# Kernel tuning notes

Hardware: AMD Instinct MI355X
Metric: run time of the kernel (lower is better)

## Reference

```python
import jax, jax.numpy as jnp
import numpy as np

LEBESGUE_P = 3          # lebesgue_p from __init__
WEIGHT_RANGE = 0.1      # weight init scale
B, C_IN, H, W = 32, 96, 56, 56
C_OUT, K = 384, 3
STRIDE = (1, 1)
PADDING = ((1, 1), (1, 1))


def setup_inputs() -> dict:
    key = jax.random.key(0)
    kx, kw = jax.random.split(key)
    x = jax.random.normal(kx, (B, C_IN, H, W), dtype=jnp.float32)
    # learned buffer 'weight': [out_channels, in_channels, kH, kW]
    weight = jax.random.normal(kw, (C_OUT, C_IN, K, K), dtype=jnp.float32) * WEIGHT_RANGE
    return {"x": x, "weight": weight}


def reference(x, weight):
    # get_pre_activations: conv with power-transformed weight sign(w)*|w|^(p-1)
    w_eff = jnp.sign(weight) * jnp.abs(weight) ** (LEBESGUE_P - 1)
    pre_x = jax.lax.conv_general_dilated(
        x, w_eff,
        window_strides=STRIDE,
        padding=PADDING,
        dimension_numbers=("NCHW", "OIHW", "NCHW"),
    )  # [B, C_OUT, H, W]

    # get_wta (groups=1): hard winner-take-all over channel dim per (b, h, w).
    # Original transposes/reshapes to [C_OUT, B*H*W], argmax over dim 0, one_hot,
    # then reshapes back; mathematically identical to a channel-axis argmax+one_hot.
    winners = jnp.argmax(pre_x, axis=1)                                   # [B, H, W]
    wta = jax.nn.one_hot(winners, pre_x.shape[1], axis=1, dtype=pre_x.dtype)  # [B, C_OUT, H, W]

    # forward(x, return_x_wta=True) returns (pre_x, wta); stack so output is one array
    return jnp.stack([pre_x, wta], axis=0)  # [2, B, C_OUT, H, W]
```

## Files before the change

### kernel.cpp

```cpp
#include <hip/hip_runtime.h>
#include <math.h>
#include <stdint.h>

#define CIN  96
#define COUT 384
#define HH   56
#define WW   56
#define BB   32

#define MARGIN   1e-3f
#define CAP      32000u
#define WT32_OFF (256 * 1024)
#define WT64_OFF (2 * 1024 * 1024)
#define WT16_OFF (5 * 1024 * 1024)
#define POSB     4

#define HL2      331776
#define XSB      6336

typedef _Float16 half8 __attribute__((ext_vector_type(8)));
typedef float    f32x4 __attribute__((ext_vector_type(4)));

template <bool WITH16>
__global__ void prep_weights(const float* __restrict__ w, float* __restrict__ wt32,
                             double* __restrict__ wt64, _Float16* __restrict__ wt16,
                             uint32_t* __restrict__ cnt) {
    int idx = blockIdx.x * blockDim.x + threadIdx.x;
    if (idx == 0) *cnt = 0u;
    if (idx >= COUT * CIN * 9) return;
    int co = idx / (CIN * 9);
    int r  = idx - co * (CIN * 9);
    double d = (double)w[idx];
    double e = d * fabs(d);
    wt64[(size_t)r * COUT + co] = e;
    float ef = (float)e;
    wt32[(size_t)r * COUT + co] = ef;
    if (WITH16) {
        _Float16 hi = (_Float16)ef;
        _Float16 lo = (_Float16)(ef - (float)hi);
        int ci  = r / 9;
        int khw = r - ci * 9;
        int off = (((co >> 4) * 12 + (ci >> 3)) * 9 + khw) * 128 + (co & 15) * 8 + (ci & 7);
        wt16[off] = hi;
        wt16[off + HL2] = lo;
    }
}

__global__ __launch_bounds__(512, 4)
void conv_mfma(const float* __restrict__ x, const _Float16* __restrict__ wt16,
               float* __restrict__ out, uint32_t* __restrict__ cnt,
               uint32_t* __restrict__ flags) {
    const int h   = blockIdx.x;
    const int b   = blockIdx.y;
    const int tid = threadIdx.x;
    const int l   = tid & 63;
    const int wg  = tid >> 6;
    const int g   = l >> 4;
    const int c   = l & 15;

    __shared__ char lds[33792];
    _Float16* xs  = (_Float16*)lds;
    float*    T   = (float*)lds;
    float4*   red = (float4*)(lds + 25344);
    int*      win = (int*)(lds + 25344 + 8192);

    f32x4 acc[4][3];
    #pragma unroll
    for (int mf = 0; mf < 4; ++mf)
        #pragma unroll
        for (int nf = 0; nf < 3; ++nf)
            #pragma unroll
            for (int q = 0; q < 4; ++q) acc[mf][nf][q] = 0.0f;

    const _Float16* pa0 = xs + (g * 198 + c) * 8;

    auto stage = [&](int chunk) {
        _Float16* xsb = xs + (chunk & 1) * XSB;
        const int ci0 = chunk * 32;
        for (int idx = tid; idx < 4 * 198; idx += 512) {
            int cq  = idx / 198;
            int rem = idx - cq * 198;
            int r   = rem / 66;
            int col = rem - r * 66;
            int gh  = h + r - 1;
            int gw  = col - 1;
            half8 hv = {};
            if ((unsigned)gh < 56u && (unsigned)gw < 56u) {
                const float* px = x + (((size_t)b * CIN + (ci0 + cq * 8)) * HH + gh) * WW + gw;
                #pragma unroll
                for (int i = 0; i < 8; ++i) hv[i] = (_Float16)px[i * 3136];
            }
            *(half8*)(xsb + (size_t)(cq * 198 + rem) * 8) = hv;
        }
    };

    stage(0);
    __syncthreads();

    for (int chunk = 0; chunk < 3; ++chunk) {
        if (chunk < 2) stage(chunk + 1);

        const _Float16* pax = pa0 + (chunk & 1) * XSB;
        const _Float16* pb0h = wt16 + (size_t)(((wg * 3 + 0) * 12 + chunk * 4 + g) * 9) * 128 + c * 8;
        const _Float16* pb1h = wt16 + (size_t)(((wg * 3 + 1) * 12 + chunk * 4 + g) * 9) * 128 + c * 8;
        const _Float16* pb2h = wt16 + (size_t)(((wg * 3 + 2) * 12 + chunk * 4 + g) * 9) * 128 + c * 8;
        const _Float16* pb0l = pb0h + HL2;
        const _Float16* pb1l = pb1h + HL2;
        const _Float16* pb2l = pb2h + HL2;

        #pragma unroll
        for (int khw = 0; khw < 9; ++khw) {
            const int kh = khw / 3;
            const int kw = khw - kh * 3;
            half8 Bh0 = *(const half8*)(pb0h + khw * 128);
            half8 Bl0 = *(const half8*)(pb0l + khw * 128);
            half8 Bh1 = *(const half8*)(pb1h + khw * 128);
            half8 Bl1 = *(const half8*)(pb1l + khw * 128);
            half8 Bh2 = *(const half8*)(pb2h + khw * 128);
            half8 Bl2 = *(const half8*)(pb2l + khw * 128);
            #pragma unroll
            for (int mf = 0; mf < 4; ++mf) {
                half8 Ah = *(const half8*)(pax + (kh * 66 + mf * 16 + kw) * 8);
                acc[mf][0] = __builtin_amdgcn_mfma_f32_16x16x32_f16(Ah, Bh0, acc[mf][0], 0, 0, 0);
                acc[mf][1] = __builtin_amdgcn_mfma_f32_16x16x32_f16(Ah, Bh1, acc[mf][1], 0, 0, 0);
                acc[mf][2] = __builtin_amdgcn_mfma_f32_16x16x32_f16(Ah, Bh2, acc[mf][2], 0, 0, 0);
                acc[mf][0] = __builtin_amdgcn_mfma_f32_16x16x32_f16(Ah, Bl0, acc[mf][0], 0, 0, 0);
                acc[mf][1] = __builtin_amdgcn_mfma_f32_16x16x32_f16(Ah, Bl1, acc[mf][1], 0, 0, 0);
                acc[mf][2] = __builtin_amdgcn_mfma_f32_16x16x32_f16(Ah, Bl2, acc[mf][2], 0, 0, 0);
            }
        }
        __syncthreads();
    }

    #pragma unroll
    for (int mf = 0; mf < 4; ++mf) {
        #pragma unroll
        for (int q = 0; q < 4; ++q) {
            float best = acc[mf][0][q];
            int   bco  = wg * 48 + c;
            float sec  = -1e30f;
            #pragma unroll
            for (int nf = 1; nf < 3; ++nf) {
                float v = acc[mf][nf][q];
                if (v > best) { sec = best; best = v; bco = wg * 48 + nf * 16 + c; }
                else if (v > sec) sec = v;
            }
            #pragma unroll
            for (int off = 1; off <= 8; off <<= 1) {
                float ov = __shfl_xor(best, off, 64);
                int   oc = __shfl_xor(bco,  off, 64);
                float os = __shfl_xor(sec,  off, 64);
                if (ov > best || (ov == best && oc < bco)) {
                    sec = fmaxf(best, os);
                    best = ov; bco = oc;
                } else {
                    sec = fmaxf(sec, ov);
                }
            }
            if (c == 0) {
                int m = mf * 16 + g * 4 + q;
                red[wg * 64 + m] = make_float4(best, sec, __int_as_float(bco), 0.0f);
            }
        }
    }
    __syncthreads();
    {
        const int m = tid >> 3;
        const int j = tid & 7;
        float4 v = red[j * 64 + m];
        float best = v.x, sec = v.y;
        int   bco  = __float_as_int(v.z);
        #pragma unroll
        for (int off = 1; off <= 4; off <<= 1) {
            float ov = __shfl_xor(best, off, 64);
            int   oc = __shfl_xor(bco,  off, 64);
            float os = __shfl_xor(sec,  off, 64);
            if (ov > best || (ov == best && oc < bco)) {
                sec = fmaxf(best, os);
                best = ov; bco = oc;
            } else {
                sec = fmaxf(sec, ov);
            }
        }
        if (j == 0 && m < 56) {
            win[m] = bco;
            if ((best - sec) < MARGIN) {
                uint32_t k = atomicAdd(cnt, 1u);
                if (k < CAP) flags[k] = (uint32_t)((b * 56 + h) * 56 + m);
            }
        }
    }
    __syncthreads();

    const size_t wta_off = (size_t)BB * COUT * HH * WW;
    for (int rnd = 0; rnd < 4; ++rnd) {
        if ((wg >> 1) == rnd) {
            const int wq = wg & 1;
            #pragma unroll
            for (int mf = 0; mf < 4; ++mf)
                #pragma unroll
                for (int nf = 0; nf < 3; ++nf)
                    #pragma unroll
                    for (int q = 0; q < 4; ++q)
                        T[(wq * 48 + nf * 16 + c) * 65 + mf * 16 + g * 4 + q] = acc[mf][nf][q];
        }
        __syncthreads();
        for (int t = tid; t < 96 * 64; t += 512) {
            int co_l = t >> 6;
            int m    = t & 63;
            if (m < 56) {
                int co  = rnd * 96 + co_l;
                float v = T[co_l * 65 + m];
                size_t o = ((size_t)(b * COUT + co)) * 3136 + (size_t)h * 56 + m;
                out[o] = v;
                out[wta_off + o] = (co == win[m]) ? 1.0f : 0.0f;
            }
        }
        __syncthreads();
    }
}

__global__ __launch_bounds__(512, 2)
void conv_wta_f32(const float* __restrict__ x, const float* __restrict__ wt,
                  float* __restrict__ out, uint32_t* __restrict__ cnt,
                  uint32_t* __restrict__ flags) {
    const int h0  = blockIdx.x * 2;
    const int b   = blockIdx.y;
    const int tid = threadIdx.x;
    const int cg  = tid & 63;
    const int wg  = tid >> 6;
    const int co0 = cg * 6;
    const int ws0 = wg * 7;

    __shared__ float xs[32 * 4 * 58];
    __shared__ int   win[2][56];

    float acc[2][6][7];
    #pragma unroll
    for (int r = 0; r < 2; ++r)
        #pragma unroll
        for (int c = 0; c < 6; ++c)
            #pragma unroll
            for (int i = 0; i < 7; ++i) acc[r][c][i] = 0.0f;

    for (int chunk = 0; chunk < 3; ++chunk) {
        const int ci0 = chunk * 32;
        __syncthreads();
        for (int idx = tid; idx < 32 * 4 * 58; idx += 512) {
            int ci  = idx / 232;
            int rem = idx - ci * 232;
            int r   = rem / 58;
            int c   = rem - r * 58;
            int gh  = h0 + r - 1;
            int gw  = c - 1;
            float v = 0.0f;
            if ((unsigned)gh < 56u && (unsigned)gw < 56u)
                v = x[(((size_t)b * CIN + (ci0 + ci)) * HH + gh) * WW + gw];
            xs[idx] = v;
        }
        __syncthreads();
        for (int ci = 0; ci < 32; ++ci) {
            const int gci = ci0 + ci;
            #pragma unroll
            for (int kh = 0; kh < 3; ++kh) {
                float xa[9], xb[9];
                const float* xr0 = &xs[(ci * 4 + kh) * 58 + ws0];
                const float* xr1 = &xs[(ci * 4 + kh + 1) * 58 + ws0];
                #pragma unroll
                for (int j = 0; j < 9; ++j) { xa[j] = xr0[j]; xb[j] = xr1[j]; }
                #pragma unroll
                for (int kw = 0; kw < 3; ++kw) {
                    const float* p = wt + (size_t)((gci * 3 + kh) * 3 + kw) * COUT + co0;
                    float2 w01 = *(const float2*)(p);
                    float2 w23 = *(const float2*)(p + 2);
                    float2 w45 = *(const float2*)(p + 4);
                    float wd[6] = {w01.x, w01.y, w23.x, w23.y, w45.x, w45.y};
                    #pragma unroll
                    for (int c = 0; c < 6; ++c)
                        #pragma unroll
                        for (int i = 0; i < 7; ++i) {
                            acc[0][c][i] = fmaf(wd[c], xa[i + kw], acc[0][c][i]);
                            acc[1][c][i] = fmaf(wd[c], xb[i + kw], acc[1][c][i]);
                        }
                }
            }
        }
    }

    #pragma unroll
    for (int rr = 0; rr < 2; ++rr) {
        #pragma unroll
        for (int i = 0; i < 7; ++i) {
            float best = acc[rr][0][i];
            int   bco  = co0;
            float sec  = -1e30f;
            #pragma unroll
            for (int c = 1; c < 6; ++c) {
                float v = acc[rr][c][i];
                if (v > best) { sec = best; best = v; bco = co0 + c; }
                else if (v > sec) sec = v;
            }
            #pragma unroll
            for (int off = 32; off > 0; off >>= 1) {
                float ov = __shfl_xor(best, off, 64);
                int   oc = __shfl_xor(bco,  off, 64);
                float os = __shfl_xor(sec,  off, 64);
                if (ov > best || (ov == best && oc < bco)) {
                    sec = fmaxf(best, os);
                    best = ov; bco = oc;
                } else {
                    sec = fmaxf(sec, ov);
                }
            }
            if (cg == 0) {
                win[rr][ws0 + i] = bco;
                if ((best - sec) < MARGIN) {
                    uint32_t k = atomicAdd(cnt, 1u);
                    if (k < CAP) flags[k] = (uint32_t)((b * 56 + (h0 + rr)) * 56 + (ws0 + i));
                }
            }
        }
    }

    const size_t wta_off = (size_t)BB * COUT * HH * WW;
    float* ldsT = xs;
    __syncthreads();
    for (int k = 0; k < 8; ++k) {
        if ((cg >> 3) == k) {
            const int cr = (cg & 7) * 6;
            #pragma unroll
            for (int c = 0; c < 6; ++c)
                #pragma unroll
                for (int rr = 0; rr < 2; ++rr)
                    #pragma unroll
                    for (int i = 0; i < 7; ++i)
                        ldsT[(cr + c) * 113 + rr * 56 + ws0 + i] = acc[rr][c][i];
        }
        __syncthreads();
        for (int l = tid; l < 48 * 112; l += 512) {
            int co_r = l / 112;
            int rem  = l - co_r * 112;
            int rr   = rem / 56;
            int w    = rem - rr * 56;
            int co   = k * 48 + co_r;
            float v  = ldsT[co_r * 113 + rem];
            size_t o = ((size_t)(b * COUT + co)) * 3136 + (size_t)(h0 + rr) * 56 + w;
            out[o] = v;
            out[wta_off + o] = (co == win[rr][w]) ? 1.0f : 0.0f;
        }
        __syncthreads();
    }
}

__global__ __launch_bounds__(384)
void fixup_f64(const float* __restrict__ x, const double* __restrict__ wt64,
               float* __restrict__ out, const uint32_t* __restrict__ cnt,
               const uint32_t* __restrict__ flags) {
    __shared__ double xp[POSB][CIN * 9];
    __shared__ double sv[POSB][COUT];
    __shared__ int winners[POSB];

    uint32_t n = *cnt;
    if (n > CAP) n = CAP;
    const int tid = threadIdx.x;
    const int wg  = tid >> 6;
    const int lane = tid & 63;
    const size_t wta_off = (size_t)BB * COUT * HH * WW;

    for (uint32_t base = blockIdx.x * POSB; base < n; base += gridDim.x * POSB) {
        int np = (int)(n - base) < POSB ? (int)(n - base) : POSB;
        __syncthreads();
        for (int idx = tid; idx < np * CIN * 9; idx += 384) {
            int p  = idx / (CIN * 9);
            int r  = idx - p * (CIN * 9);
            int ci = r / 9;
            int k  = r - ci * 9;
            int kh = k / 3, kw = k - kh * 3;
            uint32_t pos = flags[base + p];
            int w_ = pos % 56;
            int h_ = (pos / 56) % 56;
            int b_ = pos / 3136;
            int gh = h_ + kh - 1, gw = w_ + kw - 1;
            double v = 0.0;
            if ((unsigned)gh < 56u && (unsigned)gw < 56u)
                v = (double)x[(((size_t)b_ * CIN + ci) * HH + gh) * WW + gw];
            xp[p][r] = v;
        }
        __syncthreads();
        {
            const int co = tid;
            double a[POSB];
            #pragma unroll
            for (int p = 0; p < POSB; ++p) a[p] = 0.0;
            #pragma unroll 4
            for (int r = 0; r < CIN * 9; ++r) {
                double wd = wt64[(size_t)r * COUT + co];
                #pragma unroll
                for (int p = 0; p < POSB; ++p)
                    a[p] = fma(wd, xp[p][r], a[p]);
            }
            #pragma unroll
            for (int p = 0; p < POSB; ++p) sv[p][co] = a[p];
        }
        __syncthreads();
        if (wg < np) {
            double best = sv[wg][lane * 6];
            int bco = lane * 6;
            #pragma unroll
            for (int c = 1; c < 6; ++c) {
                double v2 = sv[wg][lane * 6 + c];
                if (v2 > best) { best = v2; bco = lane * 6 + c; }
            }
            #pragma unroll
            for (int off = 32; off > 0; off >>= 1) {
                double ov = __shfl_xor(best, off, 64);
                int    oc = __shfl_xor(bco,  off, 64);
                if (ov > best || (ov == best && oc < bco)) { best = ov; bco = oc; }
            }
            if (lane == 0) winners[wg] = bco;
        }
        __syncthreads();
        for (int idx = tid; idx < np * COUT; idx += 384) {
            int p  = idx / COUT;
            int co = idx - p * COUT;
            uint32_t pos = flags[base + p];
            int w_ = pos % 56;
            int h_ = (pos / 56) % 56;
            int b_ = pos / 3136;
            size_t o = (((size_t)b_ * COUT + co) * HH + h_) * WW + w_;
            out[o] = (float)sv[p][co];
            out[wta_off + o] = (co == winners[p]) ? 1.0f : 0.0f;
        }
        __syncthreads();
    }
}

__global__ __launch_bounds__(256, 2)
void conv_wta_f64(const float* __restrict__ x, const float* __restrict__ wraw,
                  float* __restrict__ out) {
    const int whalf = blockIdx.x;
    const int h     = blockIdx.y;
    const int b     = blockIdx.z;
    const int tid   = threadIdx.x;
    const int cg    = tid & 63;
    const int wg    = tid >> 6;
    const int co0   = cg * 6;
    const int wbase = whalf * 28 + wg * 7;

    __shared__ float xs[32 * 3 * 30];
    double acc[6][7];
    #pragma unroll
    for (int c = 0; c < 6; ++c)
        #pragma unroll
        for (int i = 0; i < 7; ++i) acc[c][i] = 0.0;

    for (int chunk = 0; chunk < 3; ++chunk) {
        const int ci0 = chunk * 32;
        __syncthreads();
        for (int idx = tid; idx < 32 * 3 * 30; idx += 256) {
            int ci = idx / 90, rem = idx - ci * 90;
            int r = rem / 30, c = rem - r * 30;
            int gh = h + r - 1, gw = whalf * 28 - 1 + c;
            float v = 0.0f;
            if ((unsigned)gh < 56u && (unsigned)gw < 56u)
                v = x[(((size_t)b * CIN + (ci0 + ci)) * HH + gh) * WW + gw];
            xs[idx] = v;
        }
        __syncthreads();
        for (int ci = 0; ci < 32; ++ci) {
            const int gci = ci0 + ci;
            #pragma unroll
            for (int kh = 0; kh < 3; ++kh) {
                double xd[9];
                #pragma unroll
                for (int j = 0; j < 9; ++j)
                    xd[j] = (double)xs[(ci * 3 + kh) * 30 + wg * 7 + j];
                #pragma unroll
                for (int kw = 0; kw < 3; ++kw) {
                    #pragma unroll
                    for (int c = 0; c < 6; ++c) {
                        double d = (double)wraw[(size_t)(co0 + c) * (CIN * 9) + gci * 9 + kh * 3 + kw];
                        double wd = d * fabs(d);
                        #pragma unroll
                        for (int i = 0; i < 7; ++i)
                            acc[c][i] = fma(wd, xd[i + kw], acc[c][i]);
                    }
                }
            }
        }
    }
    const size_t wta_off = (size_t)BB * COUT * HH * WW;
    #pragma unroll
    for (int i = 0; i < 7; ++i) {
        double best = acc[0][i];
        int bco = co0;
        #pragma unroll
        for (int c = 1; c < 6; ++c)
            if (acc[c][i] > best) { best = acc[c][i]; bco = co0 + c; }
        #pragma unroll
        for (int off = 32; off > 0; off >>= 1) {
            double ov = __shfl_xor(best, off, 64);
            int    oc = __shfl_xor(bco,  off, 64);
            if (ov > best || (ov == best && oc < bco)) { best = ov; bco = oc; }
        }
        const int w = wbase + i;
        #pragma unroll
        for (int c = 0; c < 6; ++c) {
            size_t o = (((size_t)b * COUT + (co0 + c)) * HH + h) * WW + w;
            out[o] = (float)acc[c][i];
            out[wta_off + o] = (co0 + c == bco) ? 1.0f : 0.0f;
        }
    }
}

extern "C" void kernel_launch(void* const* d_in, const int* in_sizes, int n_in,
                              void* d_out, int out_size, void* d_ws, size_t ws_size,
                              hipStream_t stream) {
    (void)in_sizes; (void)n_in; (void)out_size;
    const float* x = (const float*)d_in[0];
    const float* w = (const float*)d_in[1];
    float* out = (float*)d_out;

    const size_t need16 = (size_t)WT16_OFF + (size_t)2 * HL2 * sizeof(_Float16);
    const size_t need64 = (size_t)WT64_OFF + (size_t)COUT * CIN * 9 * sizeof(double);

    uint32_t* cnt   = (uint32_t*)d_ws;
    uint32_t* flags = (uint32_t*)((char*)d_ws + 256);
    float*    wt32  = (float*)((char*)d_ws + WT32_OFF);
    double*   wt64  = (double*)((char*)d_ws + WT64_OFF);
    _Float16* wt16  = (_Float16*)((char*)d_ws + WT16_OFF);

    if (ws_size >= need16) {
        prep_weights<true><<<(COUT * CIN * 9 + 255) / 256, 256, 0, stream>>>(w, wt32, wt64, wt16, cnt);
        conv_mfma<<<dim3(56, 32), 512, 0, stream>>>(x, wt16, out, cnt, flags);
        fixup_f64<<<256, 384, 0, stream>>>(x, wt64, out, cnt, flags);
    } else if (ws_size >= need64) {
        prep_weights<false><<<(COUT * CIN * 9 + 255) / 256, 256, 0, stream>>>(w, wt32, wt64, wt16, cnt);
        conv_wta_f32<<<dim3(28, 32), 512, 0, stream>>>(x, wt32, out, cnt, flags);
        fixup_f64<<<256, 384, 0, stream>>>(x, wt64, out, cnt, flags);
    } else {
        conv_wta_f64<<<dim3(2, 56, 32), 256, 0, stream>>>(x, w, out);
    }
}
```

Before: 362.8 us.

## Drop low-half fp16 weight MFMAs, prefetch B, widen fixup batch

The screening MFMA loop now uses only the high fp16 weight part and drops the hi/lo split, halving the MFMA work, and it register-prefetches the next tap's weights. To make up for the lower screening precision the margin is doubled, so more positions are sent to the fp64 fixup. The fixup kernel now processes 8 positions per block with fp32 x staging in shared memory, and the winner selection loops so each wavefront can handle several positions. The risk is that many more flagged positions could overflow CAP or make the fixup dominate the runtime.

```diff
diff --git a/kernel.cpp b/kernel.cpp
--- a/kernel.cpp
+++ b/kernel.cpp
@@ -8,12 +8,12 @@
 #define WW   56
 #define BB   32
 
-#define MARGIN   1e-3f
+#define MARGIN   2e-3f
 #define CAP      32000u
 #define WT32_OFF (256 * 1024)
 #define WT64_OFF (2 * 1024 * 1024)
 #define WT16_OFF (5 * 1024 * 1024)
-#define POSB     4
+#define POSB     8
 
 #define HL2      331776
 #define XSB      6336
@@ -101,33 +101,32 @@
         if (chunk < 2) stage(chunk + 1);
 
         const _Float16* pax = pa0 + (chunk & 1) * XSB;
-        const _Float16* pb0h = wt16 + (size_t)(((wg * 3 + 0) * 12 + chunk * 4 + g) * 9) * 128 + c * 8;
-        const _Float16* pb1h = wt16 + (size_t)(((wg * 3 + 1) * 12 + chunk * 4 + g) * 9) * 128 + c * 8;
-        const _Float16* pb2h = wt16 + (size_t)(((wg * 3 + 2) * 12 + chunk * 4 + g) * 9) * 128 + c * 8;
-        const _Float16* pb0l = pb0h + HL2;
-        const _Float16* pb1l = pb1h + HL2;
-        const _Float16* pb2l = pb2h + HL2;
+        const _Float16* pb0 = wt16 + (size_t)(((wg * 3 + 0) * 12 + chunk * 4 + g) * 9) * 128 + c * 8;
+        const _Float16* pb1 = wt16 + (size_t)(((wg * 3 + 1) * 12 + chunk * 4 + g) * 9) * 128 + c * 8;
+        const _Float16* pb2 = wt16 + (size_t)(((wg * 3 + 2) * 12 + chunk * 4 + g) * 9) * 128 + c * 8;
+
+        half8 B0 = *(const half8*)(pb0);
+        half8 B1 = *(const half8*)(pb1);
+        half8 B2 = *(const half8*)(pb2);
 
         #pragma unroll
         for (int khw = 0; khw < 9; ++khw) {
             const int kh = khw / 3;
             const int kw = khw - kh * 3;
-            half8 Bh0 = *(const half8*)(pb0h + khw * 128);
-            half8 Bl0 = *(const half8*)(pb0l + khw * 128);
-            half8 Bh1 = *(const half8*)(pb1h + khw * 128);
-            half8 Bl1 = *(const half8*)(pb1l + khw * 128);
-            half8 Bh2 = *(const half8*)(pb2h + khw * 128);
-            half8 Bl2 = *(const half8*)(pb2l + khw * 128);
+            half8 Bn0, Bn1, Bn2;
+            if (khw < 8) {
+                Bn0 = *(const half8*)(pb0 + (khw + 1) * 128);
+                Bn1 = *(const half8*)(pb1 + (khw + 1) * 128);
+                Bn2 = *(const half8*)(pb2 + (khw + 1) * 128);
+            }
             #pragma unroll
             for (int mf = 0; mf < 4; ++mf) {
                 half8 Ah = *(const half8*)(pax + (kh * 66 + mf * 16 + kw) * 8);
-                acc[mf][0] = __builtin_amdgcn_mfma_f32_16x16x32_f16(Ah, Bh0, acc[mf][0], 0, 0, 0);
-                acc[mf][1] = __builtin_amdgcn_mfma_f32_16x16x32_f16(Ah, Bh1, acc[mf][1], 0, 0, 0);
-                acc[mf][2] = __builtin_amdgcn_mfma_f32_16x16x32_f16(Ah, Bh2, acc[mf][2], 0, 0, 0);
-                acc[mf][0] = __builtin_amdgcn_mfma_f32_16x16x32_f16(Ah, Bl0, acc[mf][0], 0, 0, 0);
-                acc[mf][1] = __builtin_amdgcn_mfma_f32_16x16x32_f16(Ah, Bl1, acc[mf][1], 0, 0, 0);
-                acc[mf][2] = __builtin_amdgcn_mfma_f32_16x16x32_f16(Ah, Bl2, acc[mf][2], 0, 0, 0);
-            }
+                acc[mf][0] = __builtin_amdgcn_mfma_f32_16x16x32_f16(Ah, B0, acc[mf][0], 0, 0, 0);
+                acc[mf][1] = __builtin_amdgcn_mfma_f32_16x16x32_f16(Ah, B1, acc[mf][1], 0, 0, 0);
+                acc[mf][2] = __builtin_amdgcn_mfma_f32_16x16x32_f16(Ah, B2, acc[mf][2], 0, 0, 0);
+            }
+            if (khw < 8) { B0 = Bn0; B1 = Bn1; B2 = Bn2; }
         }
         __syncthreads();
     }
@@ -356,7 +355,7 @@
 void fixup_f64(const float* __restrict__ x, const double* __restrict__ wt64,
                float* __restrict__ out, const uint32_t* __restrict__ cnt,
                const uint32_t* __restrict__ flags) {
-    __shared__ double xp[POSB][CIN * 9];
+    __shared__ float  xp[POSB][CIN * 9];
     __shared__ double sv[POSB][COUT];
     __shared__ int winners[POSB];
 
@@ -381,9 +380,9 @@
             int h_ = (pos / 56) % 56;
             int b_ = pos / 3136;
             int gh = h_ + kh - 1, gw = w_ + kw - 1;
-            double v = 0.0;
+            float v = 0.0f;
             if ((unsigned)gh < 56u && (unsigned)gw < 56u)
-                v = (double)x[(((size_t)b_ * CIN + ci) * HH + gh) * WW + gw];
+                v = x[(((size_t)b_ * CIN + ci) * HH + gh) * WW + gw];
             xp[p][r] = v;
         }
         __syncthreads();
@@ -397,18 +396,18 @@
                 double wd = wt64[(size_t)r * COUT + co];
                 #pragma unroll
                 for (int p = 0; p < POSB; ++p)
-                    a[p] = fma(wd, xp[p][r], a[p]);
+                    a[p] = fma(wd, (double)xp[p][r], a[p]);
             }
             #pragma unroll
             for (int p = 0; p < POSB; ++p) sv[p][co] = a[p];
         }
         __syncthreads();
-        if (wg < np) {
-            double best = sv[wg][lane * 6];
+        for (int p = wg; p < np; p += 6) {
+            double best = sv[p][lane * 6];
             int bco = lane * 6;
             #pragma unroll
             for (int c = 1; c < 6; ++c) {
-                double v2 = sv[wg][lane * 6 + c];
+                double v2 = sv[p][lane * 6 + c];
                 if (v2 > best) { best = v2; bco = lane * 6 + c; }
             }
             #pragma unroll
@@ -417,7 +416,7 @@
                 int    oc = __shfl_xor(bco,  off, 64);
                 if (ov > best || (ov == best && oc < bco)) { best = ov; bco = oc; }
             }
-            if (lane == 0) winners[wg] = bco;
+            if (lane == 0) winners[p] = bco;
         }
         __syncthreads();
         for (int idx = tid; idx < np * COUT; idx += 384) {
```

Result: faster. 332.2 us (-8.4%).
